# Performance work log

Hardware: AMD Instinct MI355X
Metric: run time of the kernel (lower is better)

The kernel has to match this reference:

```python
import jax, jax.numpy as jnp
import numpy as np

H, D = 4, 64          # n_heads, feats_per_head (hidden_size = H*D = 256)
NEG_SLOPE = 0.2       # DGL GATv2Conv default negative_slope

N_GT, N_UBS, N_AG = 100000, 20000, 20000
E_SEEN, E_NEAR = 320000, 160000
F_GT, F_UBS, F_AG = 8, 8, 16
HID = H * D


def _linear_params(key, fan_in, fan_out):
    kw, kb = jax.random.split(key)
    s = 1.0 / np.sqrt(fan_in)
    W = jax.random.uniform(kw, (fan_in, fan_out), jnp.float32, -s, s)
    b = jax.random.uniform(kb, (fan_out,), jnp.float32, -s, s)
    return W, b


def setup_inputs() -> dict:
    key = jax.random.key(0)
    ks = jax.random.split(key, 16)
    inp = {
        'x_gt': jax.random.normal(ks[0], (N_GT, F_GT), jnp.float32),
        'x_ubs': jax.random.normal(ks[1], (N_UBS, F_UBS), jnp.float32),
        'x_agent': jax.random.normal(ks[2], (N_AG, F_AG), jnp.float32),
        'seen_src': jax.random.randint(ks[3], (E_SEEN,), 0, N_GT, jnp.int32),
        'seen_dst': jax.random.randint(ks[4], (E_SEEN,), 0, N_AG, jnp.int32),
        'near_src': jax.random.randint(ks[5], (E_NEAR,), 0, N_UBS, jnp.int32),
        'near_dst': jax.random.randint(ks[6], (E_NEAR,), 0, N_AG, jnp.int32),
    }
    # GATv2Conv 'seen': (gt -> agent)
    inp['Ws_seen'], inp['bs_seen'] = _linear_params(ks[7], F_GT, HID)
    inp['Wd_seen'], inp['bd_seen'] = _linear_params(ks[8], F_AG, HID)
    inp['attn_seen'] = jax.random.normal(ks[9], (H, D), jnp.float32) * 0.1
    inp['Wr_seen'], inp['br_seen'] = _linear_params(ks[10], F_AG, HID)
    # GATv2Conv 'near': (ubs -> agent)
    inp['Ws_near'], inp['bs_near'] = _linear_params(ks[11], F_UBS, HID)
    inp['Wd_near'], inp['bd_near'] = _linear_params(ks[12], F_AG, HID)
    inp['attn_near'] = jax.random.normal(ks[13], (H, D), jnp.float32) * 0.1
    inp['Wr_near'], inp['br_near'] = _linear_params(ks[14], F_AG, HID)
    # aggregation MLP: Linear(2*HID, HID) + ReLU
    inp['W_aggr'], inp['b_aggr'] = _linear_params(ks[15], 2 * HID, HID)
    return inp


def _gatv2(h_src, h_dst, src, dst, Ws, bs, Wd, bd, attn, Wr, br, n_dst):
    # DGL GATv2Conv, bipartite, residual=True, allow_zero_in_degree, ReLU activation
    fs = (h_src @ Ws + bs).reshape(-1, H, D)   # [Ns,H,D]
    fd = (h_dst @ Wd + bd).reshape(-1, H, D)   # [Nd,H,D]
    e = jax.nn.leaky_relu(fs[src] + fd[dst], NEG_SLOPE)     # [E,H,D]
    scores = jnp.einsum('ehd,hd->eh', e, attn)              # [E,H]
    # edge softmax over incoming edges of each dst node
    m = jax.ops.segment_max(scores, dst, num_segments=n_dst)
    m = jnp.where(jnp.isfinite(m), m, 0.0)                  # zero-in-degree guard
    ex = jnp.exp(scores - m[dst])
    denom = jax.ops.segment_sum(ex, dst, num_segments=n_dst)
    alpha = ex / denom[dst]                                 # [E,H]
    rst = jax.ops.segment_sum(alpha[:, :, None] * fs[src], dst, num_segments=n_dst)
    rst = rst + (h_dst @ Wr + br).reshape(-1, H, D)         # residual
    return jax.nn.relu(rst).reshape(n_dst, H * D)


def reference(x_gt, x_ubs, x_agent, seen_src, seen_dst, near_src, near_dst,
              Ws_seen, bs_seen, Wd_seen, bd_seen, attn_seen, Wr_seen, br_seen,
              Ws_near, bs_near, Wd_near, bd_near, attn_near, Wr_near, br_near,
              W_aggr, b_aggr):
    n_ag = x_agent.shape[0]
    x1 = _gatv2(x_gt, x_agent, seen_src, seen_dst,
                Ws_seen, bs_seen, Wd_seen, bd_seen, attn_seen, Wr_seen, br_seen, n_ag)
    x2 = _gatv2(x_ubs, x_agent, near_src, near_dst,
                Ws_near, bs_near, Wd_near, bd_near, attn_near, Wr_near, br_near, n_ag)
    x_out = jnp.concatenate((x1, x2), axis=1)               # [N_ag, 2*HID]
    return jax.nn.relu(x_out @ W_aggr + b_aggr)             # [N_ag, HID]
```

## Files before the change

### kernel.cpp

```cpp
#include <hip/hip_runtime.h>
#include <math.h>

#define NEG 0.2f

typedef short bf16x8 __attribute__((ext_vector_type(8)));
typedef float f32x4  __attribute__((ext_vector_type(4)));

static __device__ __forceinline__ void fma4(float4& d, float s, const float4 w) {
    d.x = fmaf(s, w.x, d.x); d.y = fmaf(s, w.y, d.y);
    d.z = fmaf(s, w.z, d.z); d.w = fmaf(s, w.w, d.w);
}
static __device__ __forceinline__ float4 lrelu4(float4 a, float4 b) {
    float4 r; float v;
    v = a.x + b.x; r.x = fmaxf(v, NEG * v);
    v = a.y + b.y; r.y = fmaxf(v, NEG * v);
    v = a.z + b.z; r.z = fmaxf(v, NEG * v);
    v = a.w + b.w; r.w = fmaxf(v, NEG * v);
    return r;
}
static __device__ __forceinline__ unsigned short f2bf(float f) {
    unsigned int x = __float_as_uint(f);
    unsigned int r = (x + 0x7FFFu + ((x >> 16) & 1u)) >> 16;
    return (unsigned short)r;
}
static __device__ __forceinline__ float rlane(float v, int l) {
    return __int_as_float(__builtin_amdgcn_readlane(__float_as_int(v), l));
}

#define DPP_ADD(x, ctrl) \
    ((x) + __int_as_float(__builtin_amdgcn_update_dpp( \
        __float_as_int(x), __float_as_int(x), (ctrl), 0xF, 0xF, true)))
static __device__ __forceinline__ float rowsum16(float v) {
    v = DPP_ADD(v, 0xB1);
    v = DPP_ADD(v, 0x4E);
    v = DPP_ADD(v, 0x141);
    v = DPP_ADD(v, 0x140);
    return v;
}

__global__ void k_hist_wt(const int* __restrict__ dst_s, int Es,
                          const int* __restrict__ dst_n, int En,
                          int* __restrict__ deg_s, int* __restrict__ deg_n,
                          const float* __restrict__ W, unsigned short* __restrict__ Wt) {
    int i = blockIdx.x * 256 + threadIdx.x;
    if (i < Es) atomicAdd(&deg_s[dst_s[i]], 1);
    int j = i - Es;
    if (j >= 0 && j < En) atomicAdd(&deg_n[dst_n[j]], 1);
    if (i < 512 * 256) {
        int k = i >> 8, n = i & 255;
        Wt[(size_t)n * 512 + k] = f2bf(W[i]);
    }
}

__global__ __launch_bounds__(1024) void k_scan2(int* a, int na, int* b, int nb) {
    int* p = (blockIdx.x == 0) ? a : b;
    int n  = (blockIdx.x == 0) ? na : nb;
    __shared__ int sums[1024];
    int t = threadIdx.x;
    int C = (n + 1023) >> 10;
    int base = t * C;
    int s = 0;
    for (int j = 0; j < C; ++j) { int i = base + j; if (i < n) s += p[i]; }
    sums[t] = s;
    __syncthreads();
    for (int off = 1; off < 1024; off <<= 1) {
        int v = (t >= off) ? sums[t - off] : 0;
        __syncthreads();
        sums[t] += v;
        __syncthreads();
    }
    int run = (t == 0) ? 0 : sums[t - 1];
    for (int j = 0; j < C; ++j) {
        int i = base + j;
        if (i < n) { int v = p[i]; p[i] = run; run += v; }
    }
}

__global__ void k_scatter(const int* __restrict__ src_s, const int* __restrict__ dst_s, int Es,
                          const int* __restrict__ src_n, const int* __restrict__ dst_n, int En,
                          int* __restrict__ cur_s, int* __restrict__ cur_n,
                          int* __restrict__ csr_s, int* __restrict__ csr_n) {
    int i = blockIdx.x * 256 + threadIdx.x;
    if (i < Es) {
        int pos = atomicAdd(&cur_s[dst_s[i]], 1);
        csr_s[pos] = src_s[i];
    }
    int j = i - Es;
    if (j >= 0 && j < En) {
        int pos = atomicAdd(&cur_n[dst_n[j]], 1);
        csr_n[pos] = src_n[j];
    }
}

__global__ __launch_bounds__(256) void k_gat(
    const float* __restrict__ xsrc_s, const int* __restrict__ pfx_s, const int* __restrict__ csr_s,
    const float* __restrict__ Ws_s, const float* __restrict__ bs_s,
    const float* __restrict__ Wd_s, const float* __restrict__ bd_s,
    const float* __restrict__ at_s,
    const float* __restrict__ Wr_s, const float* __restrict__ br_s,
    const float* __restrict__ xsrc_n, const int* __restrict__ pfx_n, const int* __restrict__ csr_n,
    const float* __restrict__ Ws_n, const float* __restrict__ bs_n,
    const float* __restrict__ Wd_n, const float* __restrict__ bd_n,
    const float* __restrict__ at_n,
    const float* __restrict__ Wr_n, const float* __restrict__ br_n,
    const float* __restrict__ x_ag,
    unsigned short* __restrict__ xcat, int n_dst, int gNs)
{
    const bool seen = (int)blockIdx.x < gNs;
    const float* x_src = seen ? xsrc_s : xsrc_n;
    const int*   pfx   = seen ? pfx_s  : pfx_n;
    const int*   csr   = seen ? csr_s  : csr_n;
    const float* Ws    = seen ? Ws_s   : Ws_n;
    const float* bs    = seen ? bs_s   : bs_n;
    const float* Wd    = seen ? Wd_s   : Wd_n;
    const float* bd    = seen ? bd_s   : bd_n;
    const float* at    = seen ? at_s   : at_n;
    const float* Wr    = seen ? Wr_s   : Wr_n;
    const float* br    = seen ? br_s   : br_n;
    const int col = seen ? 0 : 256;
    const int blk = seen ? (int)blockIdx.x : (int)blockIdx.x - gNs;

    const int t = threadIdx.x;
    const int wave = t >> 6, lane = t & 63;
    const int d0 = lane * 4;

    int gnode = blk * 16 + ((lane >> 4) << 2) + wave;
    int gn = (gnode < n_dst) ? gnode : (n_dst - 1);
    float xag = x_ag[(size_t)gn * 16 + (lane & 15)];

    int e_start[4], e_end[4];
#pragma unroll
    for (int j = 0; j < 4; ++j) {
        int nd = blk * 16 + j * 4 + wave;
        nd = (nd < n_dst) ? nd : (n_dst - 1);
        e_end[j]   = pfx[nd];
        e_start[j] = nd ? pfx[nd - 1] : 0;
    }

    float4 fd4[4], fr4[4];
    {
        const float4 bdv = *(const float4*)&bd[d0];
        const float4 brv = *(const float4*)&br[d0];
#pragma unroll
        for (int j = 0; j < 4; ++j) { fd4[j] = bdv; fr4[j] = brv; }
#pragma unroll
        for (int k = 0; k < 16; ++k) {
            float4 wd = *(const float4*)&Wd[k * 256 + d0];
            float4 wr = *(const float4*)&Wr[k * 256 + d0];
#pragma unroll
            for (int j = 0; j < 4; ++j) {
                float xk = rlane(xag, j * 16 + k);
                fma4(fd4[j], xk, wd);
                fma4(fr4[j], xk, wr);
            }
        }
    }

    float4 ws_r[8];
#pragma unroll
    for (int k = 0; k < 8; ++k) ws_r[k] = *(const float4*)&Ws[k * 256 + d0];
    const float4 bsv = *(const float4*)&bs[d0];
    const float4 atv = *(const float4*)&at[d0];

#pragma unroll
    for (int rep = 0; rep < 4; ++rep) {
        const int node = blk * 16 + rep * 4 + wave;
        if (node >= n_dst) continue;

        const int start = e_start[rep];
        const int deg   = e_end[rep] - start;
        const float4 fd = fd4[rep];
        const float4 fr = fr4[rep];

        float l = 0.f;
        float4 acc = make_float4(0.f, 0.f, 0.f, 0.f);

        if (deg > 0) {
            const int g  = lane >> 3;
            const int w8 = lane & 7;

            int e0 = (g < deg) ? g : deg - 1;
            int i0 = csr[start + e0];
            float r0 = x_src[(size_t)i0 * 8 + w8];
            int e1 = (8 + g < deg) ? 8 + g : deg - 1;
            int i1 = csr[start + e1];

            for (int base = 0; base < deg; base += 8) {
                float r1 = x_src[(size_t)i1 * 8 + w8];
                int e2 = base + 16 + g; e2 = (e2 < deg) ? e2 : deg - 1;
                int i2 = csr[start + e2];

#pragma unroll
                for (int j = 0; j < 8; ++j) {
                    if (base + j < deg) {
                        float x0 = rlane(r0, j * 8 + 0);
                        float x1 = rlane(r0, j * 8 + 1);
                        float x2 = rlane(r0, j * 8 + 2);
                        float x3 = rlane(r0, j * 8 + 3);
                        float x4 = rlane(r0, j * 8 + 4);
                        float x5 = rlane(r0, j * 8 + 5);
                        float x6 = rlane(r0, j * 8 + 6);
                        float x7 = rlane(r0, j * 8 + 7);

                        float4 fs = bsv;
                        fma4(fs, x0, ws_r[0]);
                        fma4(fs, x1, ws_r[1]);
                        fma4(fs, x2, ws_r[2]);
                        fma4(fs, x3, ws_r[3]);
                        fma4(fs, x4, ws_r[4]);
                        fma4(fs, x5, ws_r[5]);
                        fma4(fs, x6, ws_r[6]);
                        fma4(fs, x7, ws_r[7]);

                        float4 tt = lrelu4(fs, fd);
                        float sc = tt.x * atv.x;
                        sc = fmaf(tt.y, atv.y, sc);
                        sc = fmaf(tt.z, atv.z, sc);
                        sc = fmaf(tt.w, atv.w, sc);
                        sc = rowsum16(sc);

                        float p = __expf(sc);
                        l += p;
                        acc.x = fmaf(p, fs.x, acc.x);
                        acc.y = fmaf(p, fs.y, acc.y);
                        acc.z = fmaf(p, fs.z, acc.z);
                        acc.w = fmaf(p, fs.w, acc.w);
                    }
                }
                r0 = r1; i1 = i2;
            }
        }

        float inv = (l > 0.f) ? 1.f / l : 0.f;
        ushort4 o;
        o.x = f2bf(fmaxf(fmaf(acc.x, inv, fr.x), 0.f));
        o.y = f2bf(fmaxf(fmaf(acc.y, inv, fr.y), 0.f));
        o.z = f2bf(fmaxf(fmaf(acc.z, inv, fr.z), 0.f));
        o.w = f2bf(fmaxf(fmaf(acc.w, inv, fr.w), 0.f));
        *(ushort4*)&xcat[(size_t)node * 512 + col + d0] = o;
    }
}

__global__ __launch_bounds__(256) void k_mlp(
    const unsigned short* __restrict__ X, const unsigned short* __restrict__ Wt,
    const float* __restrict__ b, float* __restrict__ out, int M)
{
    const int t = threadIdx.x;
    const int wave = t >> 6, lane = t & 63;
    const int m16 = lane & 15, q = lane >> 4;
    const int rbase = blockIdx.x * 16;
    const int nbase = wave * 64;

    int rowa = rbase + m16; if (rowa >= M) rowa = M - 1;
    const unsigned short* xp = X + (size_t)rowa * 512 + q * 8;
    const unsigned short* w0 = Wt + (size_t)(nbase + m16) * 512 + q * 8;
    const unsigned short* w1 = w0 + 16 * 512;
    const unsigned short* w2 = w0 + 32 * 512;
    const unsigned short* w3 = w0 + 48 * 512;

    f32x4 ac0 = {0.f, 0.f, 0.f, 0.f}, ac1 = ac0, ac2 = ac0, ac3 = ac0;

#pragma unroll
    for (int k0 = 0; k0 < 512; k0 += 32) {
        bf16x8 a  = *(const bf16x8*)(xp + k0);
        bf16x8 b0 = *(const bf16x8*)(w0 + k0);
        bf16x8 b1 = *(const bf16x8*)(w1 + k0);
        bf16x8 b2 = *(const bf16x8*)(w2 + k0);
        bf16x8 b3 = *(const bf16x8*)(w3 + k0);
        ac0 = __builtin_amdgcn_mfma_f32_16x16x32_bf16(a, b0, ac0, 0, 0, 0);
        ac1 = __builtin_amdgcn_mfma_f32_16x16x32_bf16(a, b1, ac1, 0, 0, 0);
        ac2 = __builtin_amdgcn_mfma_f32_16x16x32_bf16(a, b2, ac2, 0, 0, 0);
        ac3 = __builtin_amdgcn_mfma_f32_16x16x32_bf16(a, b3, ac3, 0, 0, 0);
    }

#define EPI(AC, J) { \
        int coln = nbase + (J) * 16 + m16; \
        float bias = b[coln]; \
        _Pragma("unroll") \
        for (int r = 0; r < 4; ++r) { \
            int orow = rbase + q * 4 + r; \
            if (orow < M) \
                out[(size_t)orow * 256 + coln] = fmaxf(AC[r] + bias, 0.f); \
        } }
    EPI(ac0, 0) EPI(ac1, 1) EPI(ac2, 2) EPI(ac3, 3)
#undef EPI
}

extern "C" void kernel_launch(void* const* d_in, const int* in_sizes, int n_in,
                              void* d_out, int out_size, void* d_ws, size_t ws_size,
                              hipStream_t stream) {
    const float* x_gt   = (const float*)d_in[0];
    const float* x_ubs  = (const float*)d_in[1];
    const float* x_ag   = (const float*)d_in[2];
    const int* seen_src = (const int*)d_in[3];
    const int* seen_dst = (const int*)d_in[4];
    const int* near_src = (const int*)d_in[5];
    const int* near_dst = (const int*)d_in[6];
    const float* Ws_s = (const float*)d_in[7];  const float* bs_s = (const float*)d_in[8];
    const float* Wd_s = (const float*)d_in[9];  const float* bd_s = (const float*)d_in[10];
    const float* at_s = (const float*)d_in[11];
    const float* Wr_s = (const float*)d_in[12]; const float* br_s = (const float*)d_in[13];
    const float* Ws_n = (const float*)d_in[14]; const float* bs_n = (const float*)d_in[15];
    const float* Wd_n = (const float*)d_in[16]; const float* bd_n = (const float*)d_in[17];
    const float* at_n = (const float*)d_in[18];
    const float* Wr_n = (const float*)d_in[19]; const float* br_n = (const float*)d_in[20];
    const float* W_a  = (const float*)d_in[21]; const float* b_a  = (const float*)d_in[22];

    const int n_ag = in_sizes[2] / 16;
    const int E_s  = in_sizes[3];
    const int E_n  = in_sizes[5];

    char* ws = (char*)d_ws;
    int* cur_s = (int*)ws;              ws += (size_t)n_ag * 4;
    int* cur_n = (int*)ws;              ws += (size_t)n_ag * 4;
    int* csr_s = (int*)ws;              ws += (size_t)E_s * 4;
    int* csr_n = (int*)ws;              ws += (size_t)E_n * 4;
    unsigned short* xcat = (unsigned short*)ws;  ws += (size_t)n_ag * 512 * 2;
    unsigned short* Wt   = (unsigned short*)ws;

    hipMemsetAsync(cur_s, 0, (size_t)n_ag * 8, stream);

    int gE = (E_s + E_n + 255) / 256;
    k_hist_wt<<<gE, 256, 0, stream>>>(seen_dst, E_s, near_dst, E_n, cur_s, cur_n, W_a, Wt);
    k_scan2<<<2, 1024, 0, stream>>>(cur_s, n_ag, cur_n, n_ag);
    k_scatter<<<gE, 256, 0, stream>>>(seen_src, seen_dst, E_s, near_src, near_dst, E_n,
                                      cur_s, cur_n, csr_s, csr_n);

    int gN = (n_ag + 15) / 16;
    k_gat<<<2 * gN, 256, 0, stream>>>(
        x_gt,  cur_s, csr_s, Ws_s, bs_s, Wd_s, bd_s, at_s, Wr_s, br_s,
        x_ubs, cur_n, csr_n, Ws_n, bs_n, Wd_n, bd_n, at_n, Wr_n, br_n,
        x_ag, xcat, n_ag, gN);

    k_mlp<<<(n_ag + 15) / 16, 256, 0, stream>>>(xcat, Wt, b_a, (float*)d_out, n_ag);
}
```

Measured before the change: 314.3 us.

## Compute per-edge source projections with bf16 MFMA and aggregate in input space

Restructures the GAT kernel so each wave processes 16 edges at once. The per-edge Ws projection plus fd offset now runs through 16x16x32 bf16 MFMA instructions against a transposed, bf16-packed Ws held in shared memory. Softmax weights are accumulated over the 8-dim raw source features rather than the 256-dim projected features, and the projection is applied once per node at the end (linearity). This removes the per-edge scalar FMA chain and readlane broadcasts. In exchange it rounds inputs and weights to bf16 in the score path and adds shared-memory staging, a block barrier and lane shuffles.

```diff
diff --git a/kernel.cpp b/kernel.cpp
--- a/kernel.cpp
+++ b/kernel.cpp
@@ -9,14 +9,6 @@
 static __device__ __forceinline__ void fma4(float4& d, float s, const float4 w) {
     d.x = fmaf(s, w.x, d.x); d.y = fmaf(s, w.y, d.y);
     d.z = fmaf(s, w.z, d.z); d.w = fmaf(s, w.w, d.w);
-}
-static __device__ __forceinline__ float4 lrelu4(float4 a, float4 b) {
-    float4 r; float v;
-    v = a.x + b.x; r.x = fmaxf(v, NEG * v);
-    v = a.y + b.y; r.y = fmaxf(v, NEG * v);
-    v = a.z + b.z; r.z = fmaxf(v, NEG * v);
-    v = a.w + b.w; r.w = fmaxf(v, NEG * v);
-    return r;
 }
 static __device__ __forceinline__ unsigned short f2bf(float f) {
     unsigned int x = __float_as_uint(f);
@@ -26,7 +18,6 @@
 static __device__ __forceinline__ float rlane(float v, int l) {
     return __int_as_float(__builtin_amdgcn_readlane(__float_as_int(v), l));
 }
-
 #define DPP_ADD(x, ctrl) \
     ((x) + __int_as_float(__builtin_amdgcn_update_dpp( \
         __float_as_int(x), __float_as_int(x), (ctrl), 0xF, 0xF, true)))
@@ -106,6 +97,10 @@
     const float* __restrict__ x_ag,
     unsigned short* __restrict__ xcat, int n_dst, int gNs)
 {
+    __shared__ __align__(16) unsigned short sWsT[257 * 8];
+    __shared__ __align__(16) float sFD[16][256];
+    __shared__ __align__(16) float sFR[16][256];
+
     const bool seen = (int)blockIdx.x < gNs;
     const float* x_src = seen ? xsrc_s : xsrc_n;
     const int*   pfx   = seen ? pfx_s  : pfx_n;
@@ -122,27 +117,33 @@
 
     const int t = threadIdx.x;
     const int wave = t >> 6, lane = t & 63;
+    const int c = lane & 15, qv = lane >> 4;
     const int d0 = lane * 4;
 
-    int gnode = blk * 16 + ((lane >> 4) << 2) + wave;
-    int gn = (gnode < n_dst) ? gnode : (n_dst - 1);
-    float xag = x_ag[(size_t)gn * 16 + (lane & 15)];
-
-    int e_start[4], e_end[4];
-#pragma unroll
-    for (int j = 0; j < 4; ++j) {
-        int nd = blk * 16 + j * 4 + wave;
-        nd = (nd < n_dst) ? nd : (n_dst - 1);
-        e_end[j]   = pfx[nd];
-        e_start[j] = nd ? pfx[nd - 1] : 0;
-    }
-
-    float4 fd4[4], fr4[4];
     {
-        const float4 bdv = *(const float4*)&bd[d0];
-        const float4 brv = *(const float4*)&br[d0];
-#pragma unroll
-        for (int j = 0; j < 4; ++j) { fd4[j] = bdv; fr4[j] = brv; }
+        unsigned int pk[4];
+#pragma unroll
+        for (int h = 0; h < 4; ++h) {
+            unsigned int lo = f2bf(Ws[(2 * h)     * 256 + t]);
+            unsigned int hi = f2bf(Ws[(2 * h + 1) * 256 + t]);
+            pk[h] = lo | (hi << 16);
+        }
+        *(uint4*)&sWsT[t * 8] = make_uint4(pk[0], pk[1], pk[2], pk[3]);
+        if (t == 0) *(uint4*)&sWsT[256 * 8] = make_uint4(0u, 0u, 0u, 0u);
+    }
+
+    const int nodeBase = blk * 16 + wave * 4;
+    {
+        int gn = nodeBase + qv; gn = (gn < n_dst) ? gn : n_dst - 1;
+        float xag = x_ag[(size_t)gn * 16 + c];
+        float4 bdv = *(const float4*)&bd[d0];
+        float4 brv = *(const float4*)&br[d0];
+        float4 bsv4 = *(const float4*)&bs[d0];
+        float4 off0 = make_float4(bdv.x + bsv4.x, bdv.y + bsv4.y,
+                                  bdv.z + bsv4.z, bdv.w + bsv4.w);
+        float4 fd4[4], fr4[4];
+#pragma unroll
+        for (int j = 0; j < 4; ++j) { fd4[j] = off0; fr4[j] = brv; }
 #pragma unroll
         for (int k = 0; k < 16; ++k) {
             float4 wd = *(const float4*)&Wd[k * 256 + d0];
@@ -154,90 +155,121 @@
                 fma4(fr4[j], xk, wr);
             }
         }
-    }
-
-    float4 ws_r[8];
-#pragma unroll
-    for (int k = 0; k < 8; ++k) ws_r[k] = *(const float4*)&Ws[k * 256 + d0];
+#pragma unroll
+        for (int j = 0; j < 4; ++j) {
+            *(float4*)&sFD[wave * 4 + j][d0] = fd4[j];
+            *(float4*)&sFR[wave * 4 + j][d0] = fr4[j];
+        }
+    }
+    __syncthreads();
+
+    const int bzero = (qv == 0) ? 0 : 256 * 8;
+
+    float atC[16];
+#pragma unroll
+    for (int T = 0; T < 16; ++T) atC[T] = at[T * 16 + c];
     const float4 bsv = *(const float4*)&bs[d0];
-    const float4 atv = *(const float4*)&at[d0];
-
-#pragma unroll
+
+    int e_start[4], e_end[4];
+#pragma unroll
+    for (int j = 0; j < 4; ++j) {
+        int nd = nodeBase + j; nd = (nd < n_dst) ? nd : n_dst - 1;
+        e_end[j]   = pfx[nd];
+        e_start[j] = nd ? pfx[nd - 1] : 0;
+    }
+
     for (int rep = 0; rep < 4; ++rep) {
-        const int node = blk * 16 + rep * 4 + wave;
-        if (node >= n_dst) continue;
-
+        const int node = nodeBase + rep;
+        if (node >= n_dst) break;
         const int start = e_start[rep];
         const int deg   = e_end[rep] - start;
-        const float4 fd = fd4[rep];
-        const float4 fr = fr4[rep];
-
-        float l = 0.f;
-        float4 acc = make_float4(0.f, 0.f, 0.f, 0.f);
-
-        if (deg > 0) {
-            const int g  = lane >> 3;
-            const int w8 = lane & 7;
-
-            int e0 = (g < deg) ? g : deg - 1;
-            int i0 = csr[start + e0];
-            float r0 = x_src[(size_t)i0 * 8 + w8];
-            int e1 = (8 + g < deg) ? 8 + g : deg - 1;
-            int i1 = csr[start + e1];
-
-            for (int base = 0; base < deg; base += 8) {
-                float r1 = x_src[(size_t)i1 * 8 + w8];
-                int e2 = base + 16 + g; e2 = (e2 < deg) ? e2 : deg - 1;
-                int i2 = csr[start + e2];
-
-#pragma unroll
-                for (int j = 0; j < 8; ++j) {
-                    if (base + j < deg) {
-                        float x0 = rlane(r0, j * 8 + 0);
-                        float x1 = rlane(r0, j * 8 + 1);
-                        float x2 = rlane(r0, j * 8 + 2);
-                        float x3 = rlane(r0, j * 8 + 3);
-                        float x4 = rlane(r0, j * 8 + 4);
-                        float x5 = rlane(r0, j * 8 + 5);
-                        float x6 = rlane(r0, j * 8 + 6);
-                        float x7 = rlane(r0, j * 8 + 7);
-
-                        float4 fs = bsv;
-                        fma4(fs, x0, ws_r[0]);
-                        fma4(fs, x1, ws_r[1]);
-                        fma4(fs, x2, ws_r[2]);
-                        fma4(fs, x3, ws_r[3]);
-                        fma4(fs, x4, ws_r[4]);
-                        fma4(fs, x5, ws_r[5]);
-                        fma4(fs, x6, ws_r[6]);
-                        fma4(fs, x7, ws_r[7]);
-
-                        float4 tt = lrelu4(fs, fd);
-                        float sc = tt.x * atv.x;
-                        sc = fmaf(tt.y, atv.y, sc);
-                        sc = fmaf(tt.z, atv.z, sc);
-                        sc = fmaf(tt.w, atv.w, sc);
-                        sc = rowsum16(sc);
-
-                        float p = __expf(sc);
-                        l += p;
-                        acc.x = fmaf(p, fs.x, acc.x);
-                        acc.y = fmaf(p, fs.y, acc.y);
-                        acc.z = fmaf(p, fs.z, acc.z);
-                        acc.w = fmaf(p, fs.w, acc.w);
-                    }
+
+        float fdC[16];
+#pragma unroll
+        for (int T = 0; T < 16; ++T) fdC[T] = sFD[wave * 4 + rep][T * 16 + c];
+
+        float acc8[8] = {0.f, 0.f, 0.f, 0.f, 0.f, 0.f, 0.f, 0.f};
+        float lq = 0.f;
+
+        for (int base = 0; base < deg; base += 16) {
+            int er = base + c; er = (er < deg) ? er : deg - 1;
+            int idx = csr[start + er];
+            const float* xr = &x_src[(size_t)idx * 8];
+            float4 xa = *(const float4*)xr;
+            float4 xb = *(const float4*)(xr + 4);
+
+            unsigned int a0 = (unsigned int)f2bf(xa.x) | ((unsigned int)f2bf(xa.y) << 16);
+            unsigned int a1 = (unsigned int)f2bf(xa.z) | ((unsigned int)f2bf(xa.w) << 16);
+            unsigned int a2 = (unsigned int)f2bf(xb.x) | ((unsigned int)f2bf(xb.y) << 16);
+            unsigned int a3 = (unsigned int)f2bf(xb.z) | ((unsigned int)f2bf(xb.w) << 16);
+            bf16x8 Af = __builtin_bit_cast(bf16x8, make_uint4(a0, a1, a2, a3));
+
+            const int dm   = deg - base - qv * 4;
+            const int srcl = (c >> 2) << 4;
+            float pm = 0.f;
+
+#pragma unroll
+            for (int h = 0; h < 4; ++h) {
+                float sc0 = 0.f, sc1 = 0.f, sc2 = 0.f, sc3 = 0.f;
+#pragma unroll
+                for (int Tw = 0; Tw < 4; ++Tw) {
+                    const int T = h * 4 + Tw;
+                    bf16x8 Bf = *(const bf16x8*)&sWsT[bzero + (qv == 0 ? (T * 16 + c) * 8 : 0)];
+                    f32x4 Cv = {fdC[T], fdC[T], fdC[T], fdC[T]};
+                    Cv = __builtin_amdgcn_mfma_f32_16x16x32_bf16(Af, Bf, Cv, 0, 0, 0);
+                    float v0 = Cv[0], v1 = Cv[1], v2 = Cv[2], v3 = Cv[3];
+                    v0 = fmaxf(v0, NEG * v0); sc0 = fmaf(v0, atC[T], sc0);
+                    v1 = fmaxf(v1, NEG * v1); sc1 = fmaf(v1, atC[T], sc1);
+                    v2 = fmaxf(v2, NEG * v2); sc2 = fmaf(v2, atC[T], sc2);
+                    v3 = fmaxf(v3, NEG * v3); sc3 = fmaf(v3, atC[T], sc3);
                 }
-                r0 = r1; i1 = i2;
+                sc0 = rowsum16(sc0);
+                sc1 = rowsum16(sc1);
+                sc2 = rowsum16(sc2);
+                sc3 = rowsum16(sc3);
+
+                float p0 = __expf(dm > 0 ? sc0 : -1e30f);
+                float p1 = __expf(dm > 1 ? sc1 : -1e30f);
+                float p2 = __expf(dm > 2 ? sc2 : -1e30f);
+                float p3 = __expf(dm > 3 ? sc3 : -1e30f);
+
+                float g0 = __shfl(p0, srcl), g1 = __shfl(p1, srcl);
+                float g2 = __shfl(p2, srcl), g3 = __shfl(p3, srcl);
+                float s01 = (c & 1) ? g1 : g0;
+                float s23 = (c & 1) ? g3 : g2;
+                float routed = (c & 2) ? s23 : s01;
+                pm = (qv == h) ? routed : pm;
             }
+
+            lq += pm;
+            acc8[0] = fmaf(pm, xa.x, acc8[0]);
+            acc8[1] = fmaf(pm, xa.y, acc8[1]);
+            acc8[2] = fmaf(pm, xa.z, acc8[2]);
+            acc8[3] = fmaf(pm, xa.w, acc8[3]);
+            acc8[4] = fmaf(pm, xb.x, acc8[4]);
+            acc8[5] = fmaf(pm, xb.y, acc8[5]);
+            acc8[6] = fmaf(pm, xb.z, acc8[6]);
+            acc8[7] = fmaf(pm, xb.w, acc8[7]);
         }
 
+        float l = rowsum16(lq);
         float inv = (l > 0.f) ? 1.f / l : 0.f;
-        ushort4 o;
-        o.x = f2bf(fmaxf(fmaf(acc.x, inv, fr.x), 0.f));
-        o.y = f2bf(fmaxf(fmaf(acc.y, inv, fr.y), 0.f));
-        o.z = f2bf(fmaxf(fmaf(acc.z, inv, fr.z), 0.f));
-        o.w = f2bf(fmaxf(fmaf(acc.w, inv, fr.w), 0.f));
-        *(ushort4*)&xcat[(size_t)node * 512 + col + d0] = o;
+        float ok  = (l > 0.f) ? 1.f : 0.f;
+#pragma unroll
+        for (int j = 0; j < 8; ++j) acc8[j] = rowsum16(acc8[j] * inv);
+
+        float4 o = *(const float4*)&sFR[wave * 4 + rep][d0];
+        fma4(o, ok, bsv);
+#pragma unroll
+        for (int k = 0; k < 8; ++k)
+            fma4(o, acc8[k], *(const float4*)&Ws[k * 256 + d0]);
+
+        ushort4 u;
+        u.x = f2bf(fmaxf(o.x, 0.f));
+        u.y = f2bf(fmaxf(o.y, 0.f));
+        u.z = f2bf(fmaxf(o.z, 0.f));
+        u.w = f2bf(fmaxf(o.w, 0.f));
+        *(ushort4*)&xcat[(size_t)node * 512 + col + d0] = u;
     }
 }
 
```

After: 321.7 us. +2.4%, slower.
